# Kernel tuning notes

Hardware: AMD Instinct MI355X
Metric: run time of the kernel (lower is better)

Reference implementation:

```python
import jax, jax.numpy as jnp
import numpy as np

E, N, D, H, K, S = 800000, 50000, 96, 8, 12, 32  # edges, nodes, dim, heads, head_dim, edge_scalar_dim


def smooth_leaky_relu(x, a=0.2):
    # equiformer SmoothLeakyReLU: (1+a)/2 * x + (1-a)/2 * x * (2*sigmoid(x) - 1)
    return ((1 + a) / 2) * x + ((1 - a) / 2) * x * (2 * jax.nn.sigmoid(x) - 1)


def setup_inputs() -> dict:
    key = jax.random.key(0)
    ks = jax.random.split(key, 16)
    inv = lambda n: 1.0 / np.sqrt(n)
    return {
        "message": jax.random.normal(ks[0], (E, D), jnp.float32),
        "edge_attr": jax.random.normal(ks[1], (E, 1), jnp.float32),
        "edge_scalars": jax.random.normal(ks[2], (E, S), jnp.float32),
        "W_rad1": jax.random.normal(ks[3], (S, S), jnp.float32) * inv(S),
        "b_rad1": jnp.zeros((S,), jnp.float32),
        "W_rad2": jax.random.normal(ks[4], (S, D), jnp.float32) * inv(S),
        "b_rad2": jnp.zeros((D,), jnp.float32),
        "W_alpha": jax.random.normal(ks[5], (D, D), jnp.float32) * inv(D),
        "W_lin": jax.random.normal(ks[6], (D, D), jnp.float32) * inv(D),
        "w_dtp2": jax.random.normal(ks[7], (D,), jnp.float32),
        "W_lin2": jax.random.normal(ks[8], (D, D), jnp.float32) * inv(D),
        "alpha_dot": jax.random.normal(ks[9], (H, K), jnp.float32) * inv(K),
        "W_proj": jax.random.normal(ks[10], (D, D), jnp.float32) * inv(D),
        "edge_dst": jnp.sort(jax.random.randint(ks[11], (E,), 0, N)),
        "n_nodes_dst": N,
    }


def reference(message, edge_attr, edge_scalars, W_rad1, b_rad1, W_rad2, b_rad2,
              W_alpha, W_lin, w_dtp2, W_lin2, alpha_dot, W_proj,
              edge_dst, n_nodes_dst):
    # sep_act.dtp_rad: radial MLP on edge scalars -> depthwise TP weights [E, D]
    weight = jax.nn.silu(edge_scalars @ W_rad1 + b_rad1) @ W_rad2 + b_rad2
    # sep_act.dtp: depthwise tensor product (scalar irreps -> per-channel product)
    msg = message * edge_attr * weight                      # [E, D]
    # sep_alpha: LinearRS to mul_alpha scalars, split into heads
    log_alpha = (msg @ W_alpha).reshape(E, H, K)            # [E, H, K]
    # sep_act.lin + gate (scalar gate == SiLU)
    value = jax.nn.silu(msg @ W_lin)                        # [E, D]
    # sep_value: internal-weight depthwise TP + linear
    value = (value * edge_attr * w_dtp2) @ W_lin2           # [E, D]
    # attention logits
    la = smooth_leaky_relu(log_alpha)
    logits = jnp.einsum('ehk,hk->eh', la, alpha_dot)        # [E, H]
    # scatter_logsumexp over destination nodes (segment softmax)
    m = jax.ops.segment_max(logits, edge_dst, num_segments=n_nodes_dst)     # [N, H]
    z = jax.ops.segment_sum(jnp.exp(logits - m[edge_dst]), edge_dst,
                            num_segments=n_nodes_dst)
    log_Z = m + jnp.log(z)                                  # [N, H]
    alpha = jnp.exp(logits - log_Z[edge_dst])               # [E, H]
    # weighted scatter-sum aggregation
    attn = jax.ops.segment_sum(value.reshape(E, H, K) * alpha[:, :, None],
                               edge_dst, num_segments=n_nodes_dst)          # [N, H, K]
    # heads2vec + proj
    return attn.reshape(n_nodes_dst, D) @ W_proj            # [N, D]
```

## Files before the change

### kernel.cpp

```cpp
#include <hip/hip_runtime.h>
#include <math.h>

#define D 96
#define H 8
#define KH 12
#define S 32

typedef __attribute__((ext_vector_type(8))) short short8;
typedef __attribute__((ext_vector_type(4))) float f32x4;

#define MFMA(a, b, c) __builtin_amdgcn_mfma_f32_16x16x32_bf16(a, b, c, 0, 0, 0)

__device__ __forceinline__ float sigmoidf_(float x) { return 1.0f / (1.0f + __expf(-x)); }
__device__ __forceinline__ float siluf_(float x) { return x * sigmoidf_(x); }
__device__ __forceinline__ float slrelu_(float x) {
    return x * (0.2f + 0.8f * sigmoidf_(x));
}
__device__ __forceinline__ short f2bf(float f) {
    unsigned int u = __float_as_uint(f);
    u += 0x7fffu + ((u >> 16) & 1u);
    return (short)(u >> 16);
}
__device__ __forceinline__ float bf2f(ushort u) {
    return __uint_as_float(((unsigned int)u) << 16);
}

#define LDSFENCE() do { \
    asm volatile("s_waitcnt lgkmcnt(0)" ::: "memory"); \
    __builtin_amdgcn_sched_barrier(0); \
} while (0)

__global__ void pack_weights_kernel(
    const float* __restrict__ W1, const float* __restrict__ W2,
    const float* __restrict__ WA, const float* __restrict__ WL,
    const float* __restrict__ WL2, const float* __restrict__ WP,
    short* __restrict__ wB)
{
    int tid = blockIdx.x * 256 + threadIdx.x;
    if (tid >= 80 * 512) return;
    int j    = tid & 7;
    int lane = (tid >> 3) & 63;
    int fi   = tid >> 9;
    int q = lane >> 4, ln = lane & 15;
    const float* src; int ncols, tt, ff;
    if (fi < 2)       { src = W1;  ncols = 32; tt = fi;            ff = 0; }
    else if (fi < 8)  { src = W2;  ncols = 96; tt = fi - 2;        ff = 0; }
    else if (fi < 26) { src = WA;  ncols = 96; tt = (fi - 8) / 3;  ff = (fi - 8) % 3; }
    else if (fi < 44) { src = WL;  ncols = 96; tt = (fi - 26) / 3; ff = (fi - 26) % 3; }
    else if (fi < 62) { src = WL2; ncols = 96; tt = (fi - 44) / 3; ff = (fi - 44) % 3; }
    else              { src = WP;  ncols = 96; tt = (fi - 62) / 3; ff = (fi - 62) % 3; }
    int k = ff * 32 + q * 8 + j;
    int n = tt * 16 + ln;
    wB[tid] = f2bf(src[k * ncols + n]);
}

__global__ __launch_bounds__(256) void rowptr_kernel(
    const int* __restrict__ dst, int* __restrict__ rp, int E, int N)
{
    int e = blockIdx.x * 256 + threadIdx.x;
    if (e >= E) return;
    int cur  = dst[e];
    int prev = (e == 0) ? -1 : dst[e - 1];
    for (int n = prev + 1; n <= cur; n++) rp[n] = e;
    if (e == E - 1)
        for (int n = cur + 1; n <= N; n++) rp[n] = E;
}

__global__ __launch_bounds__(256, 8) void fused_edge_kernel(
    const float* __restrict__ message, const float* __restrict__ ea,
    const float* __restrict__ xs,
    const float* __restrict__ b1, const float* __restrict__ b2,
    const float* __restrict__ wdtp2, const float* __restrict__ adot,
    const short* __restrict__ wB,
    ushort* __restrict__ value, float* __restrict__ logits, int E)
{
    __shared__ __align__(16) char uni[4][3328];
    const short8* wB8 = (const short8*)wB;

    const int t    = threadIdx.x;
    const int lane = t & 63;
    const int w    = t >> 6;
    const int q    = lane >> 4;
    const int ln   = lane & 15;
    const int row0 = blockIdx.x * 64 + w * 16;

    short* sB = (short*)(uni[w]);
    float* sS = (float*)(uni[w]);

    const int Ec = E - 1;
    const int gA = min(row0 + ln, Ec);
    const int rA = ln;
    const int rC = q * 4;

    float eaR[4];
    int   gCc[4];
    bool  okC[4];
#pragma unroll
    for (int r = 0; r < 4; r++) {
        int g  = row0 + rC + r;
        okC[r] = (g < E);
        gCc[r] = min(g, Ec);
        eaR[r] = ea[gCc[r]];
    }

    {
        const float4* p = (const float4*)&xs[(size_t)gA * S + q * 8];
        float4 x0 = p[0], x1 = p[1];
        short8 af;
        af[0] = f2bf(x0.x); af[1] = f2bf(x0.y); af[2] = f2bf(x0.z); af[3] = f2bf(x0.w);
        af[4] = f2bf(x1.x); af[5] = f2bf(x1.y); af[6] = f2bf(x1.z); af[7] = f2bf(x1.w);
        f32x4 h0 = {0, 0, 0, 0}, h1 = {0, 0, 0, 0};
        h0 = MFMA(af, wB8[0 * 64 + lane], h0);
        h1 = MFMA(af, wB8[1 * 64 + lane], h1);
        float bb0 = b1[ln], bb1 = b1[16 + ln];
#pragma unroll
        for (int r = 0; r < 4; r++) {
            sB[(rC + r) * 104 + ln]      = f2bf(siluf_(h0[r] + bb0));
            sB[(rC + r) * 104 + 16 + ln] = f2bf(siluf_(h1[r] + bb1));
        }
    }

    f32x4 acc[6];
    {
        short8 hf = *(const short8*)&sB[rA * 104 + q * 8];
#pragma unroll
        for (int i = 0; i < 6; i++) acc[i] = (f32x4){0, 0, 0, 0};
#pragma unroll
        for (int i = 0; i < 6; i++) acc[i] = MFMA(hf, wB8[(2 + i) * 64 + lane], acc[i]);
    }
#pragma unroll
    for (int i = 0; i < 6; i++) {
        int n = i * 16 + ln;
        float bb = b2[n];
#pragma unroll
        for (int r = 0; r < 4; r++) {
            float mv = message[(size_t)gCc[r] * D + n];
            sB[(rC + r) * 104 + n] = f2bf(mv * eaR[r] * (acc[i][r] + bb));
        }
    }

    short8 mf0 = *(const short8*)&sB[rA * 104 + 0  + q * 8];
    short8 mf1 = *(const short8*)&sB[rA * 104 + 32 + q * 8];
    short8 mf2 = *(const short8*)&sB[rA * 104 + 64 + q * 8];
    LDSFENCE();

#pragma unroll
    for (int i = 0; i < 6; i++) acc[i] = (f32x4){0, 0, 0, 0};
#pragma unroll
    for (int i = 0; i < 6; i++) {
        acc[i] = MFMA(mf0, wB8[(8 + i * 3 + 0) * 64 + lane], acc[i]);
        acc[i] = MFMA(mf1, wB8[(8 + i * 3 + 1) * 64 + lane], acc[i]);
        acc[i] = MFMA(mf2, wB8[(8 + i * 3 + 2) * 64 + lane], acc[i]);
    }
    {
        const int rloc = lane >> 2, hh = lane & 3;
        const int gm = row0 + rloc;
        const bool ok = (gm < E);
#pragma unroll
        for (int half = 0; half < 2; half++) {
#pragma unroll
            for (int i = 0; i < 3; i++) {
                int ii = half * 3 + i;
#pragma unroll
                for (int r = 0; r < 4; r++)
                    sS[(rC + r) * 50 + i * 16 + ln] = slrelu_(acc[ii][r]);
            }
            int h = half * 4 + hh;
            float lg = 0.0f;
#pragma unroll
            for (int k = 0; k < KH; k++)
                lg += sS[rloc * 50 + hh * KH + k] * adot[h * KH + k];
            if (ok) logits[(size_t)gm * H + h] = lg;
        }
    }
    LDSFENCE();

#pragma unroll
    for (int i = 0; i < 6; i++) acc[i] = (f32x4){0, 0, 0, 0};
#pragma unroll
    for (int i = 0; i < 6; i++) {
        acc[i] = MFMA(mf0, wB8[(26 + i * 3 + 0) * 64 + lane], acc[i]);
        acc[i] = MFMA(mf1, wB8[(26 + i * 3 + 1) * 64 + lane], acc[i]);
        acc[i] = MFMA(mf2, wB8[(26 + i * 3 + 2) * 64 + lane], acc[i]);
    }
#pragma unroll
    for (int i = 0; i < 6; i++) {
        int n = i * 16 + ln;
        float wd = wdtp2[n];
#pragma unroll
        for (int r = 0; r < 4; r++)
            sB[(rC + r) * 104 + n] = f2bf(siluf_(acc[i][r]) * eaR[r] * wd);
    }

    {
        short8 vf0 = *(const short8*)&sB[rA * 104 + 0  + q * 8];
        short8 vf1 = *(const short8*)&sB[rA * 104 + 32 + q * 8];
        short8 vf2 = *(const short8*)&sB[rA * 104 + 64 + q * 8];
#pragma unroll
        for (int i = 0; i < 6; i++) acc[i] = (f32x4){0, 0, 0, 0};
#pragma unroll
        for (int i = 0; i < 6; i++) {
            acc[i] = MFMA(vf0, wB8[(44 + i * 3 + 0) * 64 + lane], acc[i]);
            acc[i] = MFMA(vf1, wB8[(44 + i * 3 + 1) * 64 + lane], acc[i]);
            acc[i] = MFMA(vf2, wB8[(44 + i * 3 + 2) * 64 + lane], acc[i]);
        }
#pragma unroll
        for (int i = 0; i < 6; i++) {
            int n = i * 16 + ln;
#pragma unroll
            for (int r = 0; r < 4; r++)
                sB[(rC + r) * 104 + n] = f2bf(acc[i][r]);
        }
        const int rloc = lane >> 2, c0 = lane & 3;
        const int gm = row0 + rloc;
        if (gm < E) {
#pragma unroll
            for (int j = 0; j < 3; j++) {
                short8 v = *(const short8*)&sB[rloc * 104 + (c0 + 4 * j) * 8];
                *(short8*)&value[(size_t)gm * D + (c0 + 4 * j) * 8] = v;
            }
        }
    }
}

__global__ __launch_bounds__(256) void node_kernel(
    const float* __restrict__ logits, const ushort* __restrict__ value,
    const int* __restrict__ rp, ushort* __restrict__ attnB, int N)
{
    const int wid  = (blockIdx.x * 256 + threadIdx.x) >> 6;
    const int lane = threadIdx.x & 63;
    if (wid >= N) return;
    const int s  = rp[wid];
    const int e1 = rp[wid + 1];

    const int h = lane & 7, eo = lane >> 3;
    float m = -INFINITY;
    for (int e = s + eo; e < e1; e += 8)
        m = fmaxf(m, logits[(size_t)e * H + h]);
    m = fmaxf(m, __shfl_xor(m, 8));
    m = fmaxf(m, __shfl_xor(m, 16));
    m = fmaxf(m, __shfl_xor(m, 32));
    float z = 0.0f;
    for (int e = s + eo; e < e1; e += 8)
        z += __expf(logits[(size_t)e * H + h] - m);
    z += __shfl_xor(z, 8);
    z += __shfl_xor(z, 16);
    z += __shfl_xor(z, 32);

    if (lane < 48) {
        const int   hc  = lane / 6;
        const float mh  = __shfl(m, hc);
        const float zv  = __shfl(z, hc);
        const float zih = (zv > 0.0f) ? (1.0f / zv) : 0.0f;
        const int c = 2 * lane;
        float a0 = 0.0f, a1 = 0.0f;
        for (int e = s; e < e1; e++) {
            float a = __expf(logits[(size_t)e * H + hc] - mh);
            unsigned v = *(const unsigned*)&value[(size_t)e * D + c];
            a0 += __uint_as_float(v << 16) * a;
            a1 += __uint_as_float(v & 0xffff0000u) * a;
        }
        unsigned lo = (unsigned)(ushort)f2bf(a0 * zih);
        unsigned hi = (unsigned)(ushort)f2bf(a1 * zih);
        *(unsigned*)&attnB[(size_t)wid * D + c] = lo | (hi << 16);
    }
}

__global__ __launch_bounds__(256) void proj_kernel(
    const ushort* __restrict__ attnB, const short* __restrict__ wB,
    float* __restrict__ out, int rows)
{
    const short8* wB8 = (const short8*)wB;
    const int t    = threadIdx.x;
    const int lane = t & 63;
    const int w    = t >> 6;
    const int q    = lane >> 4;
    const int ln   = lane & 15;
    const int row0 = blockIdx.x * 64;
    const int mA   = w * 16 + ln;
    const int gA   = row0 + mA;
    const int mC   = w * 16 + q * 4;

    short8 mf0 = {0, 0, 0, 0, 0, 0, 0, 0}, mf1 = mf0, mf2 = mf0;
    if (gA < rows) {
        mf0 = *(const short8*)&attnB[(size_t)gA * D + 0  + q * 8];
        mf1 = *(const short8*)&attnB[(size_t)gA * D + 32 + q * 8];
        mf2 = *(const short8*)&attnB[(size_t)gA * D + 64 + q * 8];
    }
    f32x4 acc[6];
#pragma unroll
    for (int i = 0; i < 6; i++) acc[i] = (f32x4){0, 0, 0, 0};
#pragma unroll
    for (int i = 0; i < 6; i++) {
        acc[i] = MFMA(mf0, wB8[(62 + i * 3 + 0) * 64 + lane], acc[i]);
        acc[i] = MFMA(mf1, wB8[(62 + i * 3 + 1) * 64 + lane], acc[i]);
        acc[i] = MFMA(mf2, wB8[(62 + i * 3 + 2) * 64 + lane], acc[i]);
    }
#pragma unroll
    for (int i = 0; i < 6; i++) {
        int nn = i * 16 + ln;
#pragma unroll
        for (int r = 0; r < 4; r++) {
            int gm = row0 + mC + r;
            if (gm < rows) out[(size_t)gm * D + nn] = acc[i][r];
        }
    }
}

extern "C" void kernel_launch(void* const* d_in, const int* in_sizes, int n_in,
                              void* d_out, int out_size, void* d_ws, size_t ws_size,
                              hipStream_t stream)
{
    const float* message      = (const float*)d_in[0];
    const float* edge_attr    = (const float*)d_in[1];
    const float* edge_scalars = (const float*)d_in[2];
    const float* W_rad1       = (const float*)d_in[3];
    const float* b_rad1       = (const float*)d_in[4];
    const float* W_rad2       = (const float*)d_in[5];
    const float* b_rad2       = (const float*)d_in[6];
    const float* W_alpha      = (const float*)d_in[7];
    const float* W_lin        = (const float*)d_in[8];
    const float* w_dtp2       = (const float*)d_in[9];
    const float* W_lin2       = (const float*)d_in[10];
    const float* alpha_dot    = (const float*)d_in[11];
    const float* W_proj       = (const float*)d_in[12];
    const int*   edge_dst     = (const int*)d_in[13];
    float* out = (float*)d_out;

    const int E = in_sizes[0] / D;
    const int N = out_size / D;

    char* p = (char*)d_ws;
    ushort* value  = (ushort*)p;  p += (size_t)E * D * 2;
    float*  logits = (float*)p;   p += (size_t)E * H * 4;
    ushort* attnB  = (ushort*)p;  p += ((size_t)N * D * 2 + 15) & ~(size_t)15;
    int*    rp     = (int*)p;     p += ((size_t)(N + 1) * 4 + 15) & ~(size_t)15;
    short*  wBuf   = (short*)p;

    pack_weights_kernel<<<(80 * 512 + 255) / 256, 256, 0, stream>>>(
        W_rad1, W_rad2, W_alpha, W_lin, W_lin2, W_proj, wBuf);
    rowptr_kernel<<<(E + 255) / 256, 256, 0, stream>>>(edge_dst, rp, E, N);
    fused_edge_kernel<<<(E + 63) / 64, 256, 0, stream>>>(
        message, edge_attr, edge_scalars, b_rad1, b_rad2, w_dtp2, alpha_dot,
        wBuf, value, logits, E);
    node_kernel<<<(N + 3) / 4, 256, 0, stream>>>(logits, value, rp, attnB, N);
    proj_kernel<<<(N + 63) / 64, 256, 0, stream>>>(attnB, wBuf, out, N);
}
```

Before: 737.0 us.

## Compute attention logits with MFMA and coalesce message loads in A-layout

```diff
diff --git a/kernel.cpp b/kernel.cpp
--- a/kernel.cpp
+++ b/kernel.cpp
@@ -1,4 +1,5 @@
 #include <hip/hip_runtime.h>
+#include <hip/hip_bf16.h>
 #include <math.h>
 
 #define D 96
@@ -17,31 +18,38 @@
     return x * (0.2f + 0.8f * sigmoidf_(x));
 }
 __device__ __forceinline__ short f2bf(float f) {
-    unsigned int u = __float_as_uint(f);
-    u += 0x7fffu + ((u >> 16) & 1u);
-    return (short)(u >> 16);
+    union { __hip_bfloat16 h; short s; } u;
+    u.h = __float2bfloat16(f);
+    return u.s;
 }
 __device__ __forceinline__ float bf2f(ushort u) {
     return __uint_as_float(((unsigned int)u) << 16);
 }
-
-#define LDSFENCE() do { \
-    asm volatile("s_waitcnt lgkmcnt(0)" ::: "memory"); \
-    __builtin_amdgcn_sched_barrier(0); \
-} while (0)
 
 __global__ void pack_weights_kernel(
     const float* __restrict__ W1, const float* __restrict__ W2,
     const float* __restrict__ WA, const float* __restrict__ WL,
     const float* __restrict__ WL2, const float* __restrict__ WP,
+    const float* __restrict__ AD,
     short* __restrict__ wB)
 {
     int tid = blockIdx.x * 256 + threadIdx.x;
-    if (tid >= 80 * 512) return;
+    if (tid >= 83 * 512) return;
     int j    = tid & 7;
     int lane = (tid >> 3) & 63;
     int fi   = tid >> 9;
     int q = lane >> 4, ln = lane & 15;
+    if (fi >= 80) {
+        int k = (fi - 80) * 32 + q * 8 + j;
+        int n = ln;
+        float v = 0.0f;
+        if (n < 8) {
+            int base = n * KH;
+            if (k >= base && k < base + KH) v = AD[n * KH + (k - base)];
+        }
+        wB[tid] = f2bf(v);
+        return;
+    }
     const float* src; int ncols, tt, ff;
     if (fi < 2)       { src = W1;  ncols = 32; tt = fi;            ff = 0; }
     else if (fi < 8)  { src = W2;  ncols = 96; tt = fi - 2;        ff = 0; }
@@ -70,11 +78,11 @@
     const float* __restrict__ message, const float* __restrict__ ea,
     const float* __restrict__ xs,
     const float* __restrict__ b1, const float* __restrict__ b2,
-    const float* __restrict__ wdtp2, const float* __restrict__ adot,
+    const float* __restrict__ wdtp2,
     const short* __restrict__ wB,
     ushort* __restrict__ value, float* __restrict__ logits, int E)
 {
-    __shared__ __align__(16) char uni[4][3328];
+    __shared__ __align__(16) short uni[4][16 * 104];
     const short8* wB8 = (const short8*)wB;
 
     const int t    = threadIdx.x;
@@ -84,8 +92,7 @@
     const int ln   = lane & 15;
     const int row0 = blockIdx.x * 64 + w * 16;
 
-    short* sB = (short*)(uni[w]);
-    float* sS = (float*)(uni[w]);
+    short* sB = uni[w];
 
     const int Ec = E - 1;
     const int gA = min(row0 + ln, Ec);
@@ -94,11 +101,9 @@
 
     float eaR[4];
     int   gCc[4];
-    bool  okC[4];
 #pragma unroll
     for (int r = 0; r < 4; r++) {
         int g  = row0 + rC + r;
-        okC[r] = (g < E);
         gCc[r] = min(g, Ec);
         eaR[r] = ea[gCc[r]];
     }
@@ -133,16 +138,31 @@
         int n = i * 16 + ln;
         float bb = b2[n];
 #pragma unroll
-        for (int r = 0; r < 4; r++) {
-            float mv = message[(size_t)gCc[r] * D + n];
-            sB[(rC + r) * 104 + n] = f2bf(mv * eaR[r] * (acc[i][r] + bb));
-        }
-    }
-
-    short8 mf0 = *(const short8*)&sB[rA * 104 + 0  + q * 8];
-    short8 mf1 = *(const short8*)&sB[rA * 104 + 32 + q * 8];
-    short8 mf2 = *(const short8*)&sB[rA * 104 + 64 + q * 8];
-    LDSFENCE();
+        for (int r = 0; r < 4; r++)
+            sB[(rC + r) * 104 + n] = f2bf(acc[i][r] + bb);
+    }
+
+    short8 mfa[3];
+    {
+        const float eaA = ea[gA];
+#pragma unroll
+        for (int f = 0; f < 3; f++) {
+            const float4* mp = (const float4*)&message[(size_t)gA * D + f * 32 + q * 8];
+            float4 m0 = mp[0], m1 = mp[1];
+            short8 wf = *(const short8*)&sB[rA * 104 + f * 32 + q * 8];
+            short8 r;
+            r[0] = f2bf(bf2f((ushort)wf[0]) * (m0.x * eaA));
+            r[1] = f2bf(bf2f((ushort)wf[1]) * (m0.y * eaA));
+            r[2] = f2bf(bf2f((ushort)wf[2]) * (m0.z * eaA));
+            r[3] = f2bf(bf2f((ushort)wf[3]) * (m0.w * eaA));
+            r[4] = f2bf(bf2f((ushort)wf[4]) * (m1.x * eaA));
+            r[5] = f2bf(bf2f((ushort)wf[5]) * (m1.y * eaA));
+            r[6] = f2bf(bf2f((ushort)wf[6]) * (m1.z * eaA));
+            r[7] = f2bf(bf2f((ushort)wf[7]) * (m1.w * eaA));
+            mfa[f] = r;
+        }
+    }
+    const short8 mf0 = mfa[0], mf1 = mfa[1], mf2 = mfa[2];
 
 #pragma unroll
     for (int i = 0; i < 6; i++) acc[i] = (f32x4){0, 0, 0, 0};
@@ -152,28 +172,29 @@
         acc[i] = MFMA(mf1, wB8[(8 + i * 3 + 1) * 64 + lane], acc[i]);
         acc[i] = MFMA(mf2, wB8[(8 + i * 3 + 2) * 64 + lane], acc[i]);
     }
-    {
-        const int rloc = lane >> 2, hh = lane & 3;
-        const int gm = row0 + rloc;
-        const bool ok = (gm < E);
-#pragma unroll
-        for (int half = 0; half < 2; half++) {
-#pragma unroll
-            for (int i = 0; i < 3; i++) {
-                int ii = half * 3 + i;
-#pragma unroll
-                for (int r = 0; r < 4; r++)
-                    sS[(rC + r) * 50 + i * 16 + ln] = slrelu_(acc[ii][r]);
+#pragma unroll
+    for (int i = 0; i < 6; i++) {
+        int n = i * 16 + ln;
+#pragma unroll
+        for (int r = 0; r < 4; r++)
+            sB[(rC + r) * 104 + n] = f2bf(slrelu_(acc[i][r]));
+    }
+    {
+        short8 la0 = *(const short8*)&sB[rA * 104 + 0  + q * 8];
+        short8 la1 = *(const short8*)&sB[rA * 104 + 32 + q * 8];
+        short8 la2 = *(const short8*)&sB[rA * 104 + 64 + q * 8];
+        f32x4 lacc = {0, 0, 0, 0};
+        lacc = MFMA(la0, wB8[80 * 64 + lane], lacc);
+        lacc = MFMA(la1, wB8[81 * 64 + lane], lacc);
+        lacc = MFMA(la2, wB8[82 * 64 + lane], lacc);
+        if (ln < 8) {
+#pragma unroll
+            for (int r = 0; r < 4; r++) {
+                int gm = row0 + rC + r;
+                if (gm < E) logits[(size_t)gm * H + ln] = lacc[r];
             }
-            int h = half * 4 + hh;
-            float lg = 0.0f;
-#pragma unroll
-            for (int k = 0; k < KH; k++)
-                lg += sS[rloc * 50 + hh * KH + k] * adot[h * KH + k];
-            if (ok) logits[(size_t)gm * H + h] = lg;
-        }
-    }
-    LDSFENCE();
+        }
+    }
 
 #pragma unroll
     for (int i = 0; i < 6; i++) acc[i] = (f32x4){0, 0, 0, 0};
@@ -337,11 +358,11 @@
     int*    rp     = (int*)p;     p += ((size_t)(N + 1) * 4 + 15) & ~(size_t)15;
     short*  wBuf   = (short*)p;
 
-    pack_weights_kernel<<<(80 * 512 + 255) / 256, 256, 0, stream>>>(
-        W_rad1, W_rad2, W_alpha, W_lin, W_lin2, W_proj, wBuf);
+    pack_weights_kernel<<<(83 * 512 + 255) / 256, 256, 0, stream>>>(
+        W_rad1, W_rad2, W_alpha, W_lin, W_lin2, W_proj, alpha_dot, wBuf);
     rowptr_kernel<<<(E + 255) / 256, 256, 0, stream>>>(edge_dst, rp, E, N);
     fused_edge_kernel<<<(E + 63) / 64, 256, 0, stream>>>(
-        message, edge_attr, edge_scalars, b_rad1, b_rad2, w_dtp2, alpha_dot,
+        message, edge_attr, edge_scalars, b_rad1, b_rad2, w_dtp2,
         wBuf, value, logits, E);
     node_kernel<<<(N + 3) / 4, 256, 0, stream>>>(logits, value, rp, attnB, N);
     proj_kernel<<<(N + 63) / 64, 256, 0, stream>>>(attnB, wBuf, out, N);
```

New measurement: 717.7 us. 1.03x faster.
